# Performance work log

Hardware: AMD Instinct MI355X
Metric: run time of the kernel (lower is better)

Reference implementation:

```python
import jax, jax.numpy as jnp
import numpy as np

N_LAYERS = 2

def setup_inputs() -> dict:
    key = jax.random.key(0)
    ks = jax.random.split(key, 11)
    B, T, S, H, V = 32, 64, 128, 1024, 32000
    dec_input = jax.random.randint(ks[0], (B, T), 0, V)
    h0 = jax.random.normal(ks[1], (N_LAYERS, B, H), jnp.float32)
    c0 = jax.random.normal(ks[2], (N_LAYERS, B, H), jnp.float32)
    encoder_outputs = jax.random.normal(ks[3], (B, S, H), jnp.float32)
    emb = jax.random.normal(ks[4], (V, H), jnp.float32) * 0.02
    emb = emb.at[0].set(0.0)  # padding_idx = 0
    W_ih = jax.random.normal(ks[5], (N_LAYERS, 4 * H, H), jnp.float32) * 0.02
    W_hh = jax.random.normal(ks[6], (N_LAYERS, 4 * H, H), jnp.float32) * 0.02
    b_ih = jax.random.normal(ks[7], (N_LAYERS, 4 * H), jnp.float32) * 0.02
    b_hh = jax.random.normal(ks[8], (N_LAYERS, 4 * H), jnp.float32) * 0.02
    cls_W = jax.random.normal(ks[9], (V, H), jnp.float32) * 0.02
    cls_b = jax.random.normal(ks[10], (V,), jnp.float32) * 0.02
    return dict(dec_input=dec_input, h0=h0, c0=c0, encoder_outputs=encoder_outputs,
                emb=emb, W_ih=W_ih, W_hh=W_hh, b_ih=b_ih, b_hh=b_hh,
                cls_W=cls_W, cls_b=cls_b)


def reference(dec_input, h0, c0, encoder_outputs, emb, W_ih, W_hh, b_ih, b_hh, cls_W, cls_b):
    # embedding (+dropout p=0) then relu, as in the torch forward
    x = jax.nn.relu(jnp.take(emb, dec_input, axis=0))  # [B,T,H]

    def step(carry, x_t):  # x_t: [B,H]
        h, c = carry  # each [L,B,H]
        inp = x_t
        new_h, new_c = [], []
        for i in range(N_LAYERS):
            gates = inp @ W_ih[i].T + b_ih[i] + h[i] @ W_hh[i].T + b_hh[i]  # [B,4H]
            ig, fg, gg, og = jnp.split(gates, 4, axis=-1)  # PyTorch LSTMCell gate order
            ci = jax.nn.sigmoid(fg) * c[i] + jax.nn.sigmoid(ig) * jnp.tanh(gg)
            hi = jax.nn.sigmoid(og) * jnp.tanh(ci)
            new_h.append(hi)
            new_c.append(ci)
            # residual (dims match since embedding_dim == rnn_dim)
            inp = hi + inp
        last = inp  # StackLSTMCell returns residual-accumulated output
        # dot attention: scores = context bmm target -> softmax (combine Linear output is discarded upstream)
        attn = jax.nn.softmax(jnp.einsum('bsh,bh->bs', encoder_outputs, last), axis=-1)
        return (jnp.stack(new_h), jnp.stack(new_c)), (last, attn)

    (hT, cT), (outs, attns) = jax.lax.scan(step, (h0, c0), jnp.swapaxes(x, 0, 1))
    outputs = jnp.swapaxes(outs, 0, 1)  # [B,T,H]
    logits = jnp.einsum('bth,vh->btv', outputs, cls_W) + cls_b  # [B,T,V]
    attn_scores = jnp.transpose(attns, (1, 2, 0))  # stack dim=2 -> [B,S,T]
    return logits, hT, cT, attn_scores
```

## Files before the change

### kernel.cpp

```cpp
#include <hip/hip_runtime.h>
#include <math.h>

typedef _Float16 f16x8 __attribute__((ext_vector_type(8)));
typedef _Float16 f16x4 __attribute__((ext_vector_type(4)));
typedef float    f32x4 __attribute__((ext_vector_type(4)));
typedef unsigned long long u64;
typedef unsigned int u32;

#define ALOAD(p)    __hip_atomic_load((p), __ATOMIC_RELAXED, __HIP_MEMORY_SCOPE_AGENT)
#define ASTORE(p,v) __hip_atomic_store((p), (v), __ATOMIC_RELAXED, __HIP_MEMORY_SCOPE_AGENT)

__global__ __launch_bounds__(256) void k_f32_to_f16(const float* __restrict__ src,
                                                    _Float16* __restrict__ dst, int n4) {
  int i = blockIdx.x * 256 + threadIdx.x;
  int stride = gridDim.x * 256;
  for (; i < n4; i += stride) {
    float4 v = ((const float4*)src)[i];
    f16x4 o;
    o.x = (_Float16)v.x; o.y = (_Float16)v.y; o.z = (_Float16)v.z; o.w = (_Float16)v.w;
    ((f16x4*)dst)[i] = o;
  }
}

__global__ __launch_bounds__(256) void k_pack0(const float* __restrict__ Whh0,
                                               _Float16* __restrict__ P) {
  int li = blockIdx.x * 256 + threadIdx.x;
  int row = li >> 7, k8 = li & 127;
  const float* s = Whh0 + (size_t)row * 1024 + k8 * 8;
  int g = row >> 10, u = row & 1023, jb = u >> 4, col = u & 15;
  int kh = k8 >> 4, rem = k8 & 15, st = rem >> 2, kslot = rem & 3;
  size_t idx = ((size_t)(((jb * 8 + kh) * 4 + st) * 4 + g)) * 64 + kslot * 16 + col;
  f16x8 o;
#pragma unroll
  for (int j = 0; j < 8; ++j) o[j] = (_Float16)s[j];
  *(f16x8*)(P + idx * 8) = o;
}

__global__ __launch_bounds__(256) void k_pack1(const float* __restrict__ Wih1,
                                               const float* __restrict__ Whh1,
                                               _Float16* __restrict__ P) {
  int li = blockIdx.x * 256 + threadIdx.x;
  int mat = li >> 19;
  int li2 = li & 524287;
  int row = li2 >> 7, k8l = li2 & 127;
  const float* s = (mat ? Whh1 : Wih1) + (size_t)row * 1024 + k8l * 8;
  int g = row >> 10, u = row & 1023, jb = u >> 4, col = u & 15;
  int k8g = mat * 128 + k8l;
  int kh = k8g >> 5, rem = k8g & 31, st = rem >> 2, kslot = rem & 3;
  size_t idx = ((size_t)(((jb * 8 + kh) * 8 + st) * 4 + g)) * 64 + kslot * 16 + col;
  f16x8 o;
#pragma unroll
  for (int j = 0; j < 8; ++j) o[j] = (_Float16)s[j];
  *(f16x8*)(P + idx * 8) = o;
}

__global__ __launch_bounds__(256) void k_embed(const int* __restrict__ dec,
                                               const float* __restrict__ emb,
                                               float* __restrict__ xf,
                                               _Float16* __restrict__ xh) {
  int i = blockIdx.x * 256 + threadIdx.x;
  int r = i >> 8;
  int c4 = i & 255;
  int b = r & 31, t = r >> 5;
  int tok = dec[b * 64 + t];
  float4 v = ((const float4*)(emb + (size_t)tok * 1024))[c4];
  v.x = fmaxf(v.x, 0.f); v.y = fmaxf(v.y, 0.f); v.z = fmaxf(v.z, 0.f); v.w = fmaxf(v.w, 0.f);
  ((float4*)(xf + (size_t)r * 1024))[c4] = v;
  f16x4 o;
  o.x = (_Float16)v.x; o.y = (_Float16)v.y; o.z = (_Float16)v.z; o.w = (_Float16)v.w;
  ((f16x4*)(xh + (size_t)r * 1024))[c4] = o;
}

__global__ __launch_bounds__(256) void k_init(const float* __restrict__ h0, const float* __restrict__ c0,
                                              float* __restrict__ c,
                                              _Float16* __restrict__ h0B, _Float16* __restrict__ h1B,
                                              int* __restrict__ bar) {
  int i = blockIdx.x * 256 + threadIdx.x;
  float hv = h0[i];
  c[i] = c0[i];
  if (i < 32768) h0B[i] = (_Float16)hv;
  else           h1B[i - 32768] = (_Float16)hv;
  if (i < 640) bar[i] = 0;
}

__global__ __launch_bounds__(256) void k_gemm0(const _Float16* __restrict__ A,
                                               const _Float16* __restrict__ Bm,
                                               const float* __restrict__ bias0,
                                               const float* __restrict__ bias1,
                                               float* __restrict__ C) {
  __shared__ _Float16 As[4 * 128 * 8];
  __shared__ _Float16 Bs[4 * 128 * 8];
  const int tid = threadIdx.x;
  const int lane = tid & 63;
  const int w = tid >> 6;
  const int wm = w >> 1, wn = w & 1;
  const _Float16* Ab = A + (size_t)blockIdx.y * 128 * 1024;
  const _Float16* Bb = Bm + (size_t)blockIdx.x * 128 * 1024;
  f32x4 acc[4][4] = {};
  for (int kc = 0; kc < 32; ++kc) {
#pragma unroll
    for (int ii = 0; ii < 2; ++ii) {
      int idx = tid + ii * 256;
      int kb = idx >> 7, row = idx & 127;
      int gofs = row * 1024 + kc * 32 + kb * 8;
      int sofs = kb * 1024 + row * 8;
      *(f16x8*)(As + sofs) = *(const f16x8*)(Ab + gofs);
      *(f16x8*)(Bs + sofs) = *(const f16x8*)(Bb + gofs);
    }
    __syncthreads();
    const int kb = lane >> 4;
    f16x8 af[4], bfv[4];
#pragma unroll
    for (int mf = 0; mf < 4; ++mf) {
      int row = wm * 64 + mf * 16 + (lane & 15);
      af[mf] = *(const f16x8*)(As + kb * 1024 + row * 8);
    }
#pragma unroll
    for (int nf = 0; nf < 4; ++nf) {
      int row = wn * 64 + nf * 16 + (lane & 15);
      bfv[nf] = *(const f16x8*)(Bs + kb * 1024 + row * 8);
    }
#pragma unroll
    for (int mf = 0; mf < 4; ++mf)
#pragma unroll
      for (int nf = 0; nf < 4; ++nf)
        acc[mf][nf] = __builtin_amdgcn_mfma_f32_16x16x32_f16(af[mf], bfv[nf], acc[mf][nf], 0, 0, 0);
    __syncthreads();
  }
  const int rl = (lane >> 4) * 4;
#pragma unroll
  for (int mf = 0; mf < 4; ++mf) {
#pragma unroll
    for (int nf = 0; nf < 4; ++nf) {
#pragma unroll
      for (int j = 0; j < 4; ++j) {
        int m = wm * 64 + mf * 16 + rl + j;
        int n = wn * 64 + nf * 16 + (lane & 15);
        int rg = blockIdx.y * 128 + m;
        int ng = blockIdx.x * 128 + n;
        C[(size_t)rg * 8192 + ng] = acc[mf][nf][j] + bias0[ng] + bias1[ng];
      }
    }
  }
}

__device__ __forceinline__ void gbar(int* bar) {
  __syncthreads();
  if (threadIdx.x == 0) {
    int* gen = bar + 544;
    int g = ALOAD(gen);
    int grp = blockIdx.x >> 3;
    int a = __hip_atomic_fetch_add(bar + grp * 32, 1, __ATOMIC_RELAXED, __HIP_MEMORY_SCOPE_AGENT);
    if (a == 7) {
      ASTORE(bar + grp * 32, 0);
      int r = __hip_atomic_fetch_add(bar + 512, 1, __ATOMIC_RELAXED, __HIP_MEMORY_SCOPE_AGENT);
      if (r == 15) {
        ASTORE(bar + 512, 0);
        ASTORE(gen, g + 1);
      }
    }
    while (ALOAD(gen) == g) __builtin_amdgcn_s_sleep(1);
  }
  __syncthreads();
}

template <int ROLE>
__device__ __forceinline__ void run_phases(
    int jb, const _Float16* __restrict__ Pk,
    const float* __restrict__ gx, const float* __restrict__ x_f,
    float* __restrict__ c_f,
    _Float16* __restrict__ h0A, _Float16* __restrict__ h0B,
    _Float16* __restrict__ h1A, _Float16* __restrict__ h1B,
    float* __restrict__ ipfA, float* __restrict__ ipfB,
    float* __restrict__ outs_f, _Float16* __restrict__ outs_h,
    float* __restrict__ outHT, float* __restrict__ outCT,
    int* bar, _Float16* As) {
  constexpr int S = ROLE ? 8 : 4;
  constexpr int NHALF = ROLE ? 2 : 1;
  constexpr int RSH = ROLE ? 8 : 7;
  constexpr int K8M = ROLE ? 255 : 127;
  const int u0 = jb * 16;
  const int tid = threadIdx.x;
  const int lane = tid & 63;
  const int kh = tid >> 6;
  const int col = lane & 15;
  const int kslot = lane >> 4;

  float* cst = c_f + ROLE * 32768;
  const float* gxbase = gx + (ROLE ? 4096 : 0);
  const int cb = tid >> 4, cul = tid & 15, cu = u0 + cul;

  const _Float16* pkbase = Pk + ((size_t)(jb * 8 + kh) * S) * 4 * 512 + lane * 8;
  const int a0off = col * 2056 + kh * S * 32 + kslot * 8;
  const int a1off = a0off + 16 * 2056;

  f16x8 wreg[S * 4];
#pragma unroll
  for (int i = 0; i < S * 4; ++i) wreg[i] = *(const f16x8*)(pkbase + i * 512);

  for (int p = 0; p <= 64; ++p) {
    const bool active = (ROLE == 0) ? (p < 64) : (p > 0);
    if (active) {
      const int t = (ROLE == 0) ? p : p - 1;
      const _Float16 *h0r, *h1r;
      _Float16 *h0w, *h1w;
      const float* ipfr; float* ipfw;
      if (p & 1) { h0r = h0A; h0w = h0B; ipfr = ipfA; ipfw = ipfB; h1r = h1B; h1w = h1A; }
      else       { h0r = h0B; h0w = h0A; ipfr = ipfB; ipfw = ipfA; h1r = h1A; h1w = h1B; }

      const float* gxr = gxbase + (size_t)(t * 32 + cb) * 8192;
      float pg0 = gxr[cu], pg1 = gxr[1024 + cu], pg2 = gxr[2048 + cu], pg3 = gxr[3072 + cu];
      float pc = cst[cb * 1024 + cu];
      float px = 0.f, pip = 0.f;
      if (ROLE == 0) px = x_f[(size_t)(t * 32 + cb) * 1024 + cu];
      else           pip = ALOAD(ipfr + cb * 1024 + cu);

#pragma unroll
      for (int hf = 0; hf < NHALF; ++hf) {
        u64 sreg[16];
#pragma unroll
        for (int i = 0; i < 8; ++i) {
          int fr = (hf * 8 + i) * 512 + tid;
          int row = fr >> RSH, k8 = fr & K8M;
          const _Float16* s;
          if (ROLE == 0) s = h0r + row * 1024 + k8 * 8;
          else           s = (k8 < 128) ? (h0r + row * 1024 + k8 * 8)
                                        : (h1r + row * 1024 + (k8 - 128) * 8);
          const u64* qq = (const u64*)s;
          sreg[2 * i]     = ALOAD(qq);
          sreg[2 * i + 1] = ALOAD(qq + 1);
        }
#pragma unroll
        for (int i = 0; i < 8; ++i) {
          int fr = (hf * 8 + i) * 512 + tid;
          int row = fr >> RSH, k8 = fr & K8M;
          u64* d = (u64*)(As + row * 2056 + k8 * 8);
          d[0] = sreg[2 * i];
          d[1] = sreg[2 * i + 1];
        }
      }
      __syncthreads();

      f32x4 acc[2][4] = {};
#pragma unroll
      for (int s2 = 0; s2 < S; ++s2) {
        f16x8 a0 = *(const f16x8*)(As + a0off + s2 * 32);
        f16x8 a1 = *(const f16x8*)(As + a1off + s2 * 32);
        acc[0][0] = __builtin_amdgcn_mfma_f32_16x16x32_f16(a0, wreg[s2 * 4 + 0], acc[0][0], 0, 0, 0);
        acc[1][0] = __builtin_amdgcn_mfma_f32_16x16x32_f16(a1, wreg[s2 * 4 + 0], acc[1][0], 0, 0, 0);
        acc[0][1] = __builtin_amdgcn_mfma_f32_16x16x32_f16(a0, wreg[s2 * 4 + 1], acc[0][1], 0, 0, 0);
        acc[1][1] = __builtin_amdgcn_mfma_f32_16x16x32_f16(a1, wreg[s2 * 4 + 1], acc[1][1], 0, 0, 0);
        acc[0][2] = __builtin_amdgcn_mfma_f32_16x16x32_f16(a0, wreg[s2 * 4 + 2], acc[0][2], 0, 0, 0);
        acc[1][2] = __builtin_amdgcn_mfma_f32_16x16x32_f16(a1, wreg[s2 * 4 + 2], acc[1][2], 0, 0, 0);
        acc[0][3] = __builtin_amdgcn_mfma_f32_16x16x32_f16(a0, wreg[s2 * 4 + 3], acc[0][3], 0, 0, 0);
        acc[1][3] = __builtin_amdgcn_mfma_f32_16x16x32_f16(a1, wreg[s2 * 4 + 3], acc[1][3], 0, 0, 0);
      }
      __syncthreads();

      float (*gs)[32][68] = (float (*)[32][68])(void*)As;
      const int rl = kslot * 4;
      if (kh < 4) {
#pragma unroll
        for (int m = 0; m < 2; ++m)
#pragma unroll
          for (int g = 0; g < 4; ++g)
#pragma unroll
            for (int j = 0; j < 4; ++j)
              gs[kh][m * 16 + rl + j][g * 16 + col] = acc[m][g][j];
      }
      __syncthreads();
      if (kh >= 4) {
#pragma unroll
        for (int m = 0; m < 2; ++m)
#pragma unroll
          for (int g = 0; g < 4; ++g)
#pragma unroll
            for (int j = 0; j < 4; ++j)
              gs[kh - 4][m * 16 + rl + j][g * 16 + col] += acc[m][g][j];
      }
      __syncthreads();

      {
        float ig = pg0, fg = pg1, gg = pg2, og = pg3;
#pragma unroll
        for (int cc = 0; cc < 4; ++cc) {
          ig += gs[cc][cb][cul];
          fg += gs[cc][cb][16 + cul];
          gg += gs[cc][cb][32 + cul];
          og += gs[cc][cb][48 + cul];
        }
        float si = 1.f / (1.f + expf(-ig));
        float sf = 1.f / (1.f + expf(-fg));
        float so = 1.f / (1.f + expf(-og));
        float ci = sf * pc + si * tanhf(gg);
        float hi = so * tanhf(ci);
        cst[cb * 1024 + cu] = ci;
        if (t == 63) {
          outHT[ROLE * 32768 + cb * 1024 + cu] = hi;
          outCT[ROLE * 32768 + cb * 1024 + cu] = ci;
        }
        if (ROLE == 0) {
          float hn = __shfl_down(hi, 1);
          float ipv = hi + px;
          float ipn = __shfl_down(ipv, 1);
          if ((cul & 1) == 0) {
            union { _Float16 h[2]; u32 v; } ph;
            ph.h[0] = (_Float16)hi; ph.h[1] = (_Float16)hn;
            ASTORE((u32*)(h0w + cb * 1024 + cu), ph.v);
            union { float f[2]; u64 v; } pi;
            pi.f[0] = ipv; pi.f[1] = ipn;
            ASTORE((u64*)(ipfw + cb * 1024 + cu), pi.v);
          }
        } else {
          float hn = __shfl_down(hi, 1);
          float ro = hi + pip;
          float rn = __shfl_down(ro, 1);
          if ((cul & 1) == 0) {
            union { _Float16 h[2]; u32 v; } ph;
            ph.h[0] = (_Float16)hi; ph.h[1] = (_Float16)hn;
            ASTORE((u32*)(h1w + cb * 1024 + cu), ph.v);
            union { _Float16 h[2]; u32 v; } po;
            po.h[0] = (_Float16)ro; po.h[1] = (_Float16)rn;
            ASTORE((u32*)(outs_h + (size_t)(t * 32 + cb) * 1024 + cu), po.v);
          }
          outs_f[(size_t)(t * 32 + cb) * 1024 + cu] = ro;
        }
      }
    }
    gbar(bar);
  }
}

__device__ __forceinline__ void conv_clsW(const float* __restrict__ src,
                                          _Float16* __restrict__ dst, int cb) {
  for (int i = cb * 512 + threadIdx.x; i < 4096000; i += 65536) {
    const float4* s = (const float4*)(src + (size_t)i * 8);
    float4 v0 = s[0], v1 = s[1];
    union { _Float16 h[8]; u64 q[2]; } o;
    o.h[0] = (_Float16)v0.x; o.h[1] = (_Float16)v0.y;
    o.h[2] = (_Float16)v0.z; o.h[3] = (_Float16)v0.w;
    o.h[4] = (_Float16)v1.x; o.h[5] = (_Float16)v1.y;
    o.h[6] = (_Float16)v1.z; o.h[7] = (_Float16)v1.w;
    u64* d = (u64*)(dst + (size_t)i * 8);
    ASTORE(d, o.q[0]);
    ASTORE(d + 1, o.q[1]);
  }
}

__device__ __forceinline__ void run_consumer(
    const _Float16* __restrict__ outs_h, const _Float16* __restrict__ clsW_h,
    const float* __restrict__ cls_b, float* __restrict__ out, int* bar, _Float16* lds) {
  __shared__ int tau_s;
  const int tid = threadIdx.x;
  const int lane = tid & 63;
  const int w = tid >> 6;
  const int wm = w >> 2, wn = w & 3;
  int* gen = bar + 544;
  int* wcnt = bar + 576;
  const int r0 = tid & 255, kb0 = tid >> 8;

  if (tid == 0) {
    while (ALOAD(bar + 608) < 128) __builtin_amdgcn_s_sleep(16);
  }
  __syncthreads();

  for (;;) {
    if (tid == 0) tau_s = __hip_atomic_fetch_add(wcnt, 1, __ATOMIC_RELAXED, __HIP_MEMORY_SCOPE_AGENT);
    __syncthreads();
    int tau = tau_s;
    if (tau >= 1000) break;
    int m = tau / 125, nt = tau - m * 125;
    if (tid == 0) {
      int need = 8 * m + 9; if (need > 65) need = 65;
      while (ALOAD(gen) < need) __builtin_amdgcn_s_sleep(64);
    }
    __syncthreads();

    const _Float16* Ab = outs_h + (size_t)m * 256 * 1024;
    const _Float16* Bb = clsW_h + (size_t)nt * 256 * 1024;
    f16x8 pa0, pa1, pb0, pb1;
    pa0 = *(const f16x8*)(Ab + r0 * 1024 + kb0 * 8);
    pa1 = *(const f16x8*)(Ab + r0 * 1024 + (kb0 + 2) * 8);
    pb0 = *(const f16x8*)(Bb + r0 * 1024 + kb0 * 8);
    pb1 = *(const f16x8*)(Bb + r0 * 1024 + (kb0 + 2) * 8);
    f32x4 acc[8][4] = {};
    for (int kc = 0; kc < 32; ++kc) {
      _Float16* Ac = lds + (kc & 1) * 8192;
      _Float16* Bc = lds + 16384 + (kc & 1) * 8192;
      *(f16x8*)(Ac + kb0 * 2048 + r0 * 8) = pa0;
      *(f16x8*)(Ac + (kb0 + 2) * 2048 + r0 * 8) = pa1;
      *(f16x8*)(Bc + kb0 * 2048 + r0 * 8) = pb0;
      *(f16x8*)(Bc + (kb0 + 2) * 2048 + r0 * 8) = pb1;
      if (kc + 1 < 32) {
        int ko = (kc + 1) * 32;
        pa0 = *(const f16x8*)(Ab + r0 * 1024 + ko + kb0 * 8);
        pa1 = *(const f16x8*)(Ab + r0 * 1024 + ko + (kb0 + 2) * 8);
        pb0 = *(const f16x8*)(Bb + r0 * 1024 + ko + kb0 * 8);
        pb1 = *(const f16x8*)(Bb + r0 * 1024 + ko + (kb0 + 2) * 8);
      }
      __syncthreads();
      const int kb = lane >> 4;
      f16x8 af[8], bf[4];
#pragma unroll
      for (int mf = 0; mf < 8; ++mf) {
        int row = wm * 128 + mf * 16 + (lane & 15);
        af[mf] = *(const f16x8*)(Ac + kb * 2048 + row * 8);
      }
#pragma unroll
      for (int nf = 0; nf < 4; ++nf) {
        int row = wn * 64 + nf * 16 + (lane & 15);
        bf[nf] = *(const f16x8*)(Bc + kb * 2048 + row * 8);
      }
#pragma unroll
      for (int mf = 0; mf < 8; ++mf)
#pragma unroll
        for (int nf = 0; nf < 4; ++nf)
          acc[mf][nf] = __builtin_amdgcn_mfma_f32_16x16x32_f16(af[mf], bf[nf], acc[mf][nf], 0, 0, 0);
    }
    const int rl = (lane >> 4) * 4;
#pragma unroll
    for (int mf = 0; mf < 8; ++mf) {
#pragma unroll
      for (int nf = 0; nf < 4; ++nf) {
#pragma unroll
        for (int j = 0; j < 4; ++j) {
          int rg = m * 256 + wm * 128 + mf * 16 + rl + j;
          int tt = rg >> 5, b = rg & 31;
          int ng = nt * 256 + wn * 64 + nf * 16 + (lane & 15);
          out[(size_t)(b * 64 + tt) * 32000 + ng] = acc[mf][nf][j] + cls_b[ng];
        }
      }
    }
  }
}

__global__ __launch_bounds__(512, 1) void k_lstm_fused(
    const _Float16* __restrict__ Pk0, const _Float16* __restrict__ Pk1,
    const float* __restrict__ gx, const float* __restrict__ x_f,
    float* __restrict__ c_f,
    _Float16* __restrict__ h0A, _Float16* __restrict__ h0B,
    _Float16* __restrict__ h1A, _Float16* __restrict__ h1B,
    float* __restrict__ ipfA, float* __restrict__ ipfB,
    float* __restrict__ outs_f, _Float16* __restrict__ outs_h,
    const float* __restrict__ cls_W, _Float16* __restrict__ clsW_h,
    const float* __restrict__ cls_b,
    float* __restrict__ out_logits,
    float* __restrict__ outHT, float* __restrict__ outCT,
    int* bar) {
  __shared__ _Float16 As[32 * 2056];
  const int bid = blockIdx.x;
  if (bid < 64) {
    run_phases<0>(bid & 63, Pk0, gx, x_f, c_f, h0A, h0B, h1A, h1B,
                  ipfA, ipfB, outs_f, outs_h, outHT, outCT, bar, As);
  } else if (bid < 128) {
    run_phases<1>(bid & 63, Pk1, gx, x_f, c_f, h0A, h0B, h1A, h1B,
                  ipfA, ipfB, outs_f, outs_h, outHT, outCT, bar, As);
  } else {
    conv_clsW(cls_W, clsW_h, bid - 128);
    __syncthreads();
    if (threadIdx.x == 0)
      __hip_atomic_fetch_add(bar + 608, 1, __ATOMIC_RELAXED, __HIP_MEMORY_SCOPE_AGENT);
  }
  run_consumer(outs_h, clsW_h, cls_b, out_logits, bar, As);
}

__global__ __launch_bounds__(256) void k_attn(const float* __restrict__ outs,
                                              const float* __restrict__ enc,
                                              float* __restrict__ att) {
  __shared__ float o_s[8][1024];
  __shared__ float sc[8][128];
  const int tid = threadIdx.x;
  const int lane = tid & 63;
  const int w = tid >> 6;
  const int b = blockIdx.x >> 3;
  const int t0 = (blockIdx.x & 7) * 8;
#pragma unroll
  for (int ii = 0; ii < 8; ++ii) {
    int idx = tid + ii * 256;
    int tt = idx >> 8, c4 = idx & 255;
    ((float4*)&o_s[tt][0])[c4] =
        *(const float4*)(outs + (size_t)((t0 + tt) * 32 + b) * 1024 + (size_t)c4 * 4);
  }
  __syncthreads();
  for (int si = 0; si < 32; ++si) {
    int s = w * 32 + si;
    float av[8] = {0, 0, 0, 0, 0, 0, 0, 0};
    const float* er = enc + (size_t)(b * 128 + s) * 1024;
#pragma unroll
    for (int i = 0; i < 4; ++i) {
      int k = i * 256 + lane * 4;
      float4 e = *(const float4*)(er + k);
#pragma unroll
      for (int tt = 0; tt < 8; ++tt) {
        float4 o = *(const float4*)&o_s[tt][k];
        av[tt] += e.x * o.x + e.y * o.y + e.z * o.z + e.w * o.w;
      }
    }
#pragma unroll
    for (int tt = 0; tt < 8; ++tt) {
      float v = av[tt];
#pragma unroll
      for (int off = 32; off > 0; off >>= 1) v += __shfl_down(v, off);
      if (lane == 0) sc[tt][s] = v;
    }
  }
  __syncthreads();
#pragma unroll
  for (int pp = 0; pp < 2; ++pp) {
    int tt = w + pp * 4;
    float a = sc[tt][lane], b2 = sc[tt][64 + lane];
    float m = fmaxf(a, b2);
#pragma unroll
    for (int off = 32; off > 0; off >>= 1) m = fmaxf(m, __shfl_xor(m, off));
    float e0 = expf(a - m), e1 = expf(b2 - m);
    float ss = e0 + e1;
#pragma unroll
    for (int off = 32; off > 0; off >>= 1) ss += __shfl_xor(ss, off);
    float r = 1.f / ss;
    att[(size_t)b * 8192 + (size_t)lane * 64 + t0 + tt] = e0 * r;
    att[(size_t)b * 8192 + (size_t)(64 + lane) * 64 + t0 + tt] = e1 * r;
  }
}

extern "C" void kernel_launch(void* const* d_in, const int* in_sizes, int n_in,
                              void* d_out, int out_size, void* d_ws, size_t ws_size,
                              hipStream_t stream) {
  const int*   dec   = (const int*)d_in[0];
  const float* h0    = (const float*)d_in[1];
  const float* c0    = (const float*)d_in[2];
  const float* enc   = (const float*)d_in[3];
  const float* emb   = (const float*)d_in[4];
  const float* W_ih  = (const float*)d_in[5];
  const float* W_hh  = (const float*)d_in[6];
  const float* b_ih  = (const float*)d_in[7];
  const float* b_hh  = (const float*)d_in[8];
  const float* cls_W = (const float*)d_in[9];
  const float* cls_b = (const float*)d_in[10];
  float* out = (float*)d_out;
  char* ws = (char*)d_ws;

  float*    x_f    = (float*)(ws + 0);
  _Float16* x_h    = (_Float16*)(ws + 8388608);
  _Float16* Pk0    = (_Float16*)(ws + 8388608);
  _Float16* Wih_h  = (_Float16*)(ws + 12582912);
  _Float16* Pk1    = (_Float16*)(ws + 29360128);
  _Float16* clsW_h = (_Float16*)(ws + 46137344);
  float*    gx     = (float*)(ws + 111673344);
  float*    outs_f = (float*)(ws + 178782208);
  _Float16* outs_h = (_Float16*)(ws + 187170816);
  float*    c_f    = (float*)(ws + 191627264);
  _Float16* h0A    = (_Float16*)(ws + 191889408);
  _Float16* h0B    = (_Float16*)(ws + 191954944);
  _Float16* h1A    = (_Float16*)(ws + 192020480);
  _Float16* h1B    = (_Float16*)(ws + 192086016);
  int*      bar    = (int*)(ws + 192151552);
  float*    ipfA   = (float*)(ws + 192155648);
  float*    ipfB   = (float*)(ws + 192286720);

  k_f32_to_f16<<<2048, 256, 0, stream>>>(W_ih, Wih_h, 2097152);
  k_embed<<<2048, 256, 0, stream>>>(dec, emb, x_f, x_h);
  k_init<<<256, 256, 0, stream>>>(h0, c0, c_f, h0B, h1B, bar);
  k_pack1<<<4096, 256, 0, stream>>>(W_ih + (size_t)4096 * 1024, W_hh + (size_t)4096 * 1024, Pk1);
  k_gemm0<<<dim3(64, 16), 256, 0, stream>>>(x_h, Wih_h, b_ih, b_hh, gx);
  k_pack0<<<2048, 256, 0, stream>>>(W_hh, Pk0);

  k_lstm_fused<<<256, 512, 0, stream>>>(Pk0, Pk1, gx, x_f, c_f,
                                        h0A, h0B, h1A, h1B, ipfA, ipfB,
                                        outs_f, outs_h, cls_W, clsW_h, cls_b, out,
                                        out + (size_t)65536000, out + (size_t)65601536,
                                        bar);

  k_attn<<<256, 256, 0, stream>>>(outs_f, enc, out + (size_t)65667072);
}
```

Measured before the change: 823.6 us.

## Use per-timestep hidden-state history buffers with plain vector loads instead of atomics

```diff
diff --git a/kernel.cpp b/kernel.cpp
--- a/kernel.cpp
+++ b/kernel.cpp
@@ -73,13 +73,13 @@
 
 __global__ __launch_bounds__(256) void k_init(const float* __restrict__ h0, const float* __restrict__ c0,
                                               float* __restrict__ c,
-                                              _Float16* __restrict__ h0B, _Float16* __restrict__ h1B,
+                                              _Float16* __restrict__ h0S, _Float16* __restrict__ h1S,
                                               int* __restrict__ bar) {
   int i = blockIdx.x * 256 + threadIdx.x;
   float hv = h0[i];
   c[i] = c0[i];
-  if (i < 32768) h0B[i] = (_Float16)hv;
-  else           h1B[i - 32768] = (_Float16)hv;
+  if (i < 32768) h0S[i] = (_Float16)hv;
+  else           h1S[i - 32768] = (_Float16)hv;
   if (i < 640) bar[i] = 0;
 }
 
@@ -169,8 +169,7 @@
     int jb, const _Float16* __restrict__ Pk,
     const float* __restrict__ gx, const float* __restrict__ x_f,
     float* __restrict__ c_f,
-    _Float16* __restrict__ h0A, _Float16* __restrict__ h0B,
-    _Float16* __restrict__ h1A, _Float16* __restrict__ h1B,
+    _Float16* __restrict__ h0S, _Float16* __restrict__ h1S,
     float* __restrict__ ipfA, float* __restrict__ ipfB,
     float* __restrict__ outs_f, _Float16* __restrict__ outs_h,
     float* __restrict__ outHT, float* __restrict__ outCT,
@@ -202,11 +201,13 @@
     const bool active = (ROLE == 0) ? (p < 64) : (p > 0);
     if (active) {
       const int t = (ROLE == 0) ? p : p - 1;
-      const _Float16 *h0r, *h1r;
-      _Float16 *h0w, *h1w;
+      const _Float16* h0r = h0S + (size_t)p * 32768;
+      _Float16* h0w = h0S + (size_t)(p + 1) * 32768;
+      const _Float16* h1r = h1S + (size_t)(p - 1) * 32768;
+      _Float16* h1w = h1S + (size_t)p * 32768;
       const float* ipfr; float* ipfw;
-      if (p & 1) { h0r = h0A; h0w = h0B; ipfr = ipfA; ipfw = ipfB; h1r = h1B; h1w = h1A; }
-      else       { h0r = h0B; h0w = h0A; ipfr = ipfB; ipfw = ipfA; h1r = h1A; h1w = h1B; }
+      if (p & 1) { ipfr = ipfA; ipfw = ipfB; }
+      else       { ipfr = ipfB; ipfw = ipfA; }
 
       const float* gxr = gxbase + (size_t)(t * 32 + cb) * 8192;
       float pg0 = gxr[cu], pg1 = gxr[1024 + cu], pg2 = gxr[2048 + cu], pg3 = gxr[3072 + cu];
@@ -217,7 +218,7 @@
 
 #pragma unroll
       for (int hf = 0; hf < NHALF; ++hf) {
-        u64 sreg[16];
+        f16x8 sreg[8];
 #pragma unroll
         for (int i = 0; i < 8; ++i) {
           int fr = (hf * 8 + i) * 512 + tid;
@@ -226,17 +227,13 @@
           if (ROLE == 0) s = h0r + row * 1024 + k8 * 8;
           else           s = (k8 < 128) ? (h0r + row * 1024 + k8 * 8)
                                         : (h1r + row * 1024 + (k8 - 128) * 8);
-          const u64* qq = (const u64*)s;
-          sreg[2 * i]     = ALOAD(qq);
-          sreg[2 * i + 1] = ALOAD(qq + 1);
+          sreg[i] = *(const f16x8*)s;
         }
 #pragma unroll
         for (int i = 0; i < 8; ++i) {
           int fr = (hf * 8 + i) * 512 + tid;
           int row = fr >> RSH, k8 = fr & K8M;
-          u64* d = (u64*)(As + row * 2056 + k8 * 8);
-          d[0] = sreg[2 * i];
-          d[1] = sreg[2 * i + 1];
+          *(f16x8*)(As + row * 2056 + k8 * 8) = sreg[i];
         }
       }
       __syncthreads();
@@ -334,8 +331,9 @@
 __device__ __forceinline__ void conv_clsW(const float* __restrict__ src,
                                           _Float16* __restrict__ dst, int cb) {
   for (int i = cb * 512 + threadIdx.x; i < 4096000; i += 65536) {
-    const float4* s = (const float4*)(src + (size_t)i * 8);
-    float4 v0 = s[0], v1 = s[1];
+    const f32x4* s = (const f32x4*)(src + (size_t)i * 8);
+    f32x4 v0 = __builtin_nontemporal_load(s);
+    f32x4 v1 = __builtin_nontemporal_load(s + 1);
     union { _Float16 h[8]; u64 q[2]; } o;
     o.h[0] = (_Float16)v0.x; o.h[1] = (_Float16)v0.y;
     o.h[2] = (_Float16)v0.z; o.h[3] = (_Float16)v0.w;
@@ -427,7 +425,8 @@
           int rg = m * 256 + wm * 128 + mf * 16 + rl + j;
           int tt = rg >> 5, b = rg & 31;
           int ng = nt * 256 + wn * 64 + nf * 16 + (lane & 15);
-          out[(size_t)(b * 64 + tt) * 32000 + ng] = acc[mf][nf][j] + cls_b[ng];
+          __builtin_nontemporal_store(acc[mf][nf][j] + cls_b[ng],
+                                      &out[(size_t)(b * 64 + tt) * 32000 + ng]);
         }
       }
     }
@@ -438,8 +437,7 @@
     const _Float16* __restrict__ Pk0, const _Float16* __restrict__ Pk1,
     const float* __restrict__ gx, const float* __restrict__ x_f,
     float* __restrict__ c_f,
-    _Float16* __restrict__ h0A, _Float16* __restrict__ h0B,
-    _Float16* __restrict__ h1A, _Float16* __restrict__ h1B,
+    _Float16* __restrict__ h0S, _Float16* __restrict__ h1S,
     float* __restrict__ ipfA, float* __restrict__ ipfB,
     float* __restrict__ outs_f, _Float16* __restrict__ outs_h,
     const float* __restrict__ cls_W, _Float16* __restrict__ clsW_h,
@@ -450,10 +448,10 @@
   __shared__ _Float16 As[32 * 2056];
   const int bid = blockIdx.x;
   if (bid < 64) {
-    run_phases<0>(bid & 63, Pk0, gx, x_f, c_f, h0A, h0B, h1A, h1B,
+    run_phases<0>(bid & 63, Pk0, gx, x_f, c_f, h0S, h1S,
                   ipfA, ipfB, outs_f, outs_h, outHT, outCT, bar, As);
   } else if (bid < 128) {
-    run_phases<1>(bid & 63, Pk1, gx, x_f, c_f, h0A, h0B, h1A, h1B,
+    run_phases<1>(bid & 63, Pk1, gx, x_f, c_f, h0S, h1S,
                   ipfA, ipfB, outs_f, outs_h, outHT, outCT, bar, As);
   } else {
     conv_clsW(cls_W, clsW_h, bid - 128);
@@ -543,29 +541,27 @@
   _Float16* x_h    = (_Float16*)(ws + 8388608);
   _Float16* Pk0    = (_Float16*)(ws + 8388608);
   _Float16* Wih_h  = (_Float16*)(ws + 12582912);
+  _Float16* h0S    = (_Float16*)(ws + 16777216);
+  _Float16* h1S    = (_Float16*)(ws + 21037056);
   _Float16* Pk1    = (_Float16*)(ws + 29360128);
   _Float16* clsW_h = (_Float16*)(ws + 46137344);
   float*    gx     = (float*)(ws + 111673344);
   float*    outs_f = (float*)(ws + 178782208);
   _Float16* outs_h = (_Float16*)(ws + 187170816);
   float*    c_f    = (float*)(ws + 191627264);
-  _Float16* h0A    = (_Float16*)(ws + 191889408);
-  _Float16* h0B    = (_Float16*)(ws + 191954944);
-  _Float16* h1A    = (_Float16*)(ws + 192020480);
-  _Float16* h1B    = (_Float16*)(ws + 192086016);
   int*      bar    = (int*)(ws + 192151552);
   float*    ipfA   = (float*)(ws + 192155648);
   float*    ipfB   = (float*)(ws + 192286720);
 
   k_f32_to_f16<<<2048, 256, 0, stream>>>(W_ih, Wih_h, 2097152);
   k_embed<<<2048, 256, 0, stream>>>(dec, emb, x_f, x_h);
-  k_init<<<256, 256, 0, stream>>>(h0, c0, c_f, h0B, h1B, bar);
   k_pack1<<<4096, 256, 0, stream>>>(W_ih + (size_t)4096 * 1024, W_hh + (size_t)4096 * 1024, Pk1);
   k_gemm0<<<dim3(64, 16), 256, 0, stream>>>(x_h, Wih_h, b_ih, b_hh, gx);
   k_pack0<<<2048, 256, 0, stream>>>(W_hh, Pk0);
+  k_init<<<256, 256, 0, stream>>>(h0, c0, c_f, h0S, h1S, bar);
 
   k_lstm_fused<<<256, 512, 0, stream>>>(Pk0, Pk1, gx, x_f, c_f,
-                                        h0A, h0B, h1A, h1B, ipfA, ipfB,
+                                        h0S, h1S, ipfA, ipfB,
                                         outs_f, outs_h, cls_W, clsW_h, cls_b, out,
                                         out + (size_t)65536000, out + (size_t)65601536,
                                         bar);
```

New measurement: 699.5 us. 15.1% less time.
